# Kernel tuning notes

Measured on AMD Instinct MI355X. Metric: run time of the kernel, lower is better.

## Reference

```python
import jax, jax.numpy as jnp
import numpy as np

NA = 100000  # number of a-type nodes (rows of adj)
NB = 100000  # number of b-type nodes (cols of adj)
NE = 1600000 # number of edges (nnz of adj)
BF = 128     # b_features
AF = 128     # a_features


def setup_inputs() -> dict:
    key = jax.random.key(0)
    k1, k2, k3, k4, k5, k6 = jax.random.split(key, 6)
    stdv = 1.0 / np.sqrt(BF)
    return {
        "b_input": jax.random.normal(k1, (NB, BF), dtype=jnp.float32),
        "edge_rows": jax.random.randint(k2, (NE,), 0, NA, dtype=jnp.int32),
        "edge_cols": jax.random.randint(k3, (NE,), 0, NB, dtype=jnp.int32),
        "edge_vals": jax.random.uniform(k4, (NE,), dtype=jnp.float32),
        "a_weight": jax.random.uniform(k5, (BF, AF), minval=-stdv, maxval=stdv, dtype=jnp.float32),
        "a_bias": jax.random.uniform(k6, (AF,), minval=-stdv, maxval=stdv, dtype=jnp.float32),
    }


def reference(b_input, edge_rows, edge_cols, edge_vals, a_weight, a_bias):
    # a_support = b_input @ a_weight            : [NB, AF]
    a_support = jnp.matmul(b_input, a_weight)
    # a_output = spmm(adj, a_support)           : [NA, AF]
    # adj[r, c] = edge_vals at (edge_rows, edge_cols)
    gathered = a_support[edge_cols] * edge_vals[:, None]   # [NE, AF]
    a_output = jax.ops.segment_sum(gathered, edge_rows, num_segments=NA)
    # bias=True -> early return of a-side output
    return a_output + a_bias
```

## Files before the change

kernel.cpp:

```cpp
#include <hip/hip_runtime.h>
#include <hip/hip_bf16.h>

#define AF 128
#define BF 128
#define BROWS 64
#define CAP_F 1600
#define SORT_CAP 2048
#define CROWS 1024
#define CAP_C 18432
#define CHUNK1 2048
#define NCOARSE_MAX 128

typedef __attribute__((ext_vector_type(8))) short bf16x8;
typedef __attribute__((ext_vector_type(4))) float f32x4;

__device__ inline unsigned short f2bf(float f) {
    unsigned int u = __float_as_uint(f);
    u += 0x7FFF + ((u >> 16) & 1);
    return (unsigned short)(u >> 16);
}
__device__ inline unsigned int pk2bf(float x, float y) {
    __hip_bfloat162 h = __float22bfloat162_rn(make_float2(x, y));
    return *(unsigned int*)&h;
}
__device__ inline float bflo(unsigned int u) { return __uint_as_float(u << 16); }
__device__ inline float bfhi(unsigned int u) { return __uint_as_float(u & 0xFFFF0000u); }

__global__ __launch_bounds__(256) void prep_kernel(const float* __restrict__ W,
                                                   unsigned short* __restrict__ Wt,
                                                   int* __restrict__ grelC,
                                                   int* __restrict__ grelF) {
    const int idx = blockIdx.x * 256 + threadIdx.x;
    const int n = idx >> 7, k = idx & 127;
    Wt[idx] = f2bf(W[(size_t)k * AF + n]);
    if (blockIdx.x == 0) {
        #pragma unroll
        for (int i = threadIdx.x; i < 1024; i += 256) grelC[i] = 0;
        #pragma unroll
        for (int i = threadIdx.x; i < 2048; i += 256) grelF[i] = 0;
    }
}

__global__ __launch_bounds__(256) void phase1_kernel(const float* __restrict__ Bin,
                                                     const unsigned short* __restrict__ Wt,
                                                     unsigned int* __restrict__ Sup, int NB,
                                                     const int* __restrict__ rows,
                                                     const int* __restrict__ cols,
                                                     const float* __restrict__ vals,
                                                     int* __restrict__ grelC,
                                                     int2* __restrict__ binnedC,
                                                     int NE, int NCOARSE, int ngemm) {
    __shared__ int h[NCOARSE_MAX];
    __shared__ int rbase[NCOARSE_MAX];
    const int tid = threadIdx.x;

    if ((int)blockIdx.x < ngemm) {
        const int lane = tid & 63;
        const int wave = tid >> 6;
        const int row0 = blockIdx.x * 64;
        const int m = lane & 15;
        const int quad = lane >> 4;

        int arow = row0 + wave * 16 + m;
        int arow_c = (arow < NB) ? arow : (NB - 1);
        const float* ap = Bin + (size_t)arow_c * BF + quad * 8;
        bf16x8 af[4];
        #pragma unroll
        for (int ks = 0; ks < 4; ks++) {
            float4 lo = *(const float4*)(ap + ks * 32);
            float4 hi = *(const float4*)(ap + ks * 32 + 4);
            union { unsigned int u[4]; bf16x8 v; } cv;
            cv.u[0] = pk2bf(lo.x, lo.y); cv.u[1] = pk2bf(lo.z, lo.w);
            cv.u[2] = pk2bf(hi.x, hi.y); cv.u[3] = pk2bf(hi.z, hi.w);
            af[ks] = cv.v;
        }

        f32x4 acc[8];
        #pragma unroll
        for (int nt = 0; nt < 8; nt++) {
            f32x4 a = {0.f, 0.f, 0.f, 0.f};
            const unsigned short* wp = Wt + (size_t)(nt * 16 + m) * 128 + quad * 8;
            #pragma unroll
            for (int ks = 0; ks < 4; ks++) {
                bf16x8 bf = *(const bf16x8*)(wp + ks * 32);
                a = __builtin_amdgcn_mfma_f32_16x16x32_bf16(af[ks], bf, a, 0, 0, 0);
            }
            acc[nt] = a;
        }
        #pragma unroll
        for (int nt = 0; nt < 4; nt++) {
            #pragma unroll
            for (int r = 0; r < 4; r++) {
                int row = row0 + wave * 16 + quad * 4 + r;
                if (row < NB)
                    Sup[(size_t)row * 64 + nt * 16 + m] = pk2bf(acc[nt][r], acc[nt + 4][r]);
            }
        }
    } else {
        int bid = blockIdx.x - ngemm;
        int base = bid * CHUNK1;
        int ke[8]; int px[8]; float pv[8];
        #pragma unroll
        for (int i = 0; i < 8; i++) {
            int e = base + tid + i * 256;
            if (e < NE) {
                int r = rows[e];
                ke[i] = r >> 10;
                px[i] = cols[e] | ((r & 1023) << 17);
                pv[i] = vals[e];
            } else ke[i] = -1;
        }
        if (tid < NCOARSE) h[tid] = 0;
        __syncthreads();
        #pragma unroll
        for (int i = 0; i < 8; i++)
            if (ke[i] >= 0) atomicAdd(&h[ke[i]], 1);
        __syncthreads();
        if (tid < NCOARSE) {
            int c = h[tid];
            rbase[tid] = tid * CAP_C + (c ? atomicAdd(&grelC[tid], c) : 0);
            h[tid] = 0;
        }
        __syncthreads();
        #pragma unroll
        for (int i = 0; i < 8; i++) {
            if (ke[i] >= 0) {
                int lp = atomicAdd(&h[ke[i]], 1);
                binnedC[rbase[ke[i]] + lp] = make_int2(px[i], __float_as_int(pv[i]));
            }
        }
    }
}

__global__ __launch_bounds__(256) void passA2_kernel(const int2* __restrict__ binnedC,
                                                     const int* __restrict__ grelC,
                                                     int* __restrict__ grelF,
                                                     int2* __restrict__ binnedF, int NBUCK) {
    __shared__ int h[16];
    __shared__ int rb[16];
    const int tid = threadIdx.x;
    const int j = blockIdx.x >> 4;
    const int s = blockIdx.x & 15;
    int n = grelC[j]; if (n > CAP_C) n = CAP_C;
    const int st = (n * s) >> 4;
    const int en = (n * (s + 1)) >> 4;
    const int2* src = binnedC + (size_t)j * CAP_C;

    int sub[5]; int qx[5]; int qy[5];
    #pragma unroll
    for (int i = 0; i < 5; i++) {
        int idx = st + tid + i * 256;
        if (idx < en) {
            int2 p = src[idx];
            sub[i] = p.x >> 23;
            qx[i] = p.x & 0x7FFFFF;
            qy[i] = p.y;
        } else sub[i] = -1;
    }
    if (tid < 16) h[tid] = 0;
    __syncthreads();
    #pragma unroll
    for (int i = 0; i < 5; i++)
        if (sub[i] >= 0) atomicAdd(&h[sub[i]], 1);
    __syncthreads();
    if (tid < 16) {
        int c = h[tid];
        int fine = j * 16 + tid;
        rb[tid] = (fine < NBUCK) ? (fine * CAP_F + (c ? atomicAdd(&grelF[fine], c) : 0)) : 0;
        h[tid] = 0;
    }
    __syncthreads();
    #pragma unroll
    for (int i = 0; i < 5; i++) {
        if (sub[i] >= 0) {
            int lp = atomicAdd(&h[sub[i]], 1);
            binnedF[(size_t)rb[sub[i]] + lp] = make_int2(qx[i], qy[i]);
        }
    }
}

__global__ __launch_bounds__(256) void spmm_sorted_kernel(const unsigned short* __restrict__ Sup,
                                                          const int2* __restrict__ binned,
                                                          const int* __restrict__ grel,
                                                          const float* __restrict__ bias,
                                                          float* __restrict__ out, int NA) {
    __shared__ int2 spxy[SORT_CAP];
    __shared__ int cnt[BROWS];
    __shared__ int rs[BROWS + 1];
    __shared__ int cur[BROWS];
    const int tid = threadIdx.x;
    const int b = blockIdx.x;
    int n = grel[b]; if (n > CAP_F) n = CAP_F;
    const int2* src = binned + (size_t)b * CAP_F;

    int2 pr[7];
    #pragma unroll
    for (int j = 0; j < 7; j++) {
        int i = tid + j * 256;
        pr[j] = (i < n) ? src[i] : make_int2(-1, 0);
    }
    if (tid < BROWS) cnt[tid] = 0;
    __syncthreads();
    #pragma unroll
    for (int j = 0; j < 7; j++)
        if (pr[j].x >= 0) atomicAdd(&cnt[(pr[j].x >> 17) & 63], 1);
    __syncthreads();
    if (tid < 64) {
        int v = (cnt[tid] + 7) & ~7;
        int x = v;
        #pragma unroll
        for (int off = 1; off < 64; off <<= 1) {
            int t = __shfl_up(x, off);
            if (tid >= off) x += t;
        }
        rs[tid] = x - v;
        cur[tid] = x - v;
        if (tid == 63) rs[64] = x;
    }
    __syncthreads();
    #pragma unroll
    for (int j = 0; j < 7; j++) {
        if (pr[j].x >= 0) {
            int lr = (pr[j].x >> 17) & 63;
            int pos = atomicAdd(&cur[lr], 1);
            spxy[pos] = make_int2(pr[j].x & 0x1FFFF, pr[j].y);
        }
    }
    __syncthreads();
    if (tid < BROWS) {
        int end = rs[tid + 1];
        for (int p = cur[tid]; p < end; p++) spxy[p] = make_int2(0, 0);
    }
    __syncthreads();

    const int lane = tid & 63;
    const int wv = tid >> 6;
    const float b0 = bias[lane];
    const float b1 = bias[64 + lane];
    int r = wv * 16;
    const int rend = r + 16;
    int e = rs[r];
    const int eend = rs[rend];
    int nb = rs[r + 1];
    float ax = 0.f, ay = 0.f;

    int2 q[8]; unsigned int su[8];
    if (e < eend) {
        #pragma unroll
        for (int t = 0; t < 8; t++) q[t] = spxy[e + t];
        #pragma unroll
        for (int t = 0; t < 8; t++)
            su[t] = *(const unsigned int*)(Sup + (size_t)q[t].x * AF + lane * 2);
    }
    while (e < eend) {
        const int en2 = e + 8;
        int2 q2[8]; unsigned int s2[8];
        if (en2 < eend) {
            #pragma unroll
            for (int t = 0; t < 8; t++) q2[t] = spxy[en2 + t];
            #pragma unroll
            for (int t = 0; t < 8; t++)
                s2[t] = *(const unsigned int*)(Sup + (size_t)q2[t].x * AF + lane * 2);
        }
        while (e >= nb) {
            int row = b * BROWS + r;
            if (row < NA) {
                out[(size_t)row * AF + lane]      = ax + b0;
                out[(size_t)row * AF + 64 + lane] = ay + b1;
            }
            ax = 0.f; ay = 0.f;
            ++r; nb = rs[r + 1];
        }
        #pragma unroll
        for (int t = 0; t < 8; t++) {
            float v = __int_as_float(q[t].y);
            ax += v * bflo(su[t]);
            ay += v * bfhi(su[t]);
        }
        #pragma unroll
        for (int t = 0; t < 8; t++) { q[t] = q2[t]; su[t] = s2[t]; }
        e = en2;
    }
    while (r < rend) {
        int row = b * BROWS + r;
        if (row < NA) {
            out[(size_t)row * AF + lane]      = ax + b0;
            out[(size_t)row * AF + 64 + lane] = ay + b1;
        }
        ax = 0.f; ay = 0.f;
        ++r;
    }
}

extern "C" void kernel_launch(void* const* d_in, const int* in_sizes, int n_in,
                              void* d_out, int out_size, void* d_ws, size_t ws_size,
                              hipStream_t stream) {
    const float* b_input   = (const float*)d_in[0];
    const int*   edge_rows = (const int*)d_in[1];
    const int*   edge_cols = (const int*)d_in[2];
    const float* edge_vals = (const float*)d_in[3];
    const float* a_weight  = (const float*)d_in[4];
    const float* a_bias    = (const float*)d_in[5];
    const int NB = in_sizes[0] / BF;
    const int NE = in_sizes[1];
    const int NA = out_size / AF;
    const int NBUCK = (NA + BROWS - 1) / BROWS;
    const int NCOARSE = (NA + CROWS - 1) / CROWS;
    float* out = (float*)d_out;

    char* ws = (char*)d_ws;
    size_t off = 0;
    unsigned short* Sup = (unsigned short*)(ws + off); off += (size_t)NB * AF * sizeof(unsigned short);
    int* grelC = (int*)(ws + off); off += 1024 * sizeof(int);
    int* grelF = (int*)(ws + off); off += 2048 * sizeof(int);
    unsigned short* Wt = (unsigned short*)(ws + off); off += (size_t)128 * 128 * sizeof(unsigned short);
    int2* binnedC = (int2*)(ws + off); off += (size_t)NCOARSE * CAP_C * sizeof(int2);
    int2* binnedF = (int2*)(ws + off); off += (size_t)NBUCK * CAP_F * sizeof(int2);
    (void)ws_size; (void)n_in;

    const int ngemm = (NB + 63) / 64;
    const int npass = (NE + CHUNK1 - 1) / CHUNK1;
    prep_kernel<<<64, 256, 0, stream>>>(a_weight, Wt, grelC, grelF);
    phase1_kernel<<<ngemm + npass, 256, 0, stream>>>(
        b_input, Wt, (unsigned int*)Sup, NB,
        edge_rows, edge_cols, edge_vals, grelC, binnedC, NE, NCOARSE, ngemm);
    passA2_kernel<<<NCOARSE * 16, 256, 0, stream>>>(binnedC, grelC, grelF, binnedF, NBUCK);
    spmm_sorted_kernel<<<NBUCK, 256, 0, stream>>>(Sup, binnedF, grelF, a_bias, out, NA);
}
```

Measured before the change: 226.1 us.

## Replace two-level edge binning with direct per-row atomic slot buckets

Instead of bucketing edges in two passes (coarse buckets, then fine 64-row buckets) and sorting them in shared memory, each edge now takes a slot in a fixed-capacity per-row buffer through a global atomic on a per-row counter. This removes the second binning kernel and the in-block counting sort. The SpMM kernel then loads each row's slots directly and accumulates eight rows per wave. In exchange it adds one global atomic per edge and reads full fixed-size row buffers even when they are mostly empty. Any edges beyond 46 per row are silently dropped.

```diff
diff --git a/kernel.cpp b/kernel.cpp
--- a/kernel.cpp
+++ b/kernel.cpp
@@ -3,13 +3,10 @@
 
 #define AF 128
 #define BF 128
-#define BROWS 64
-#define CAP_F 1600
-#define SORT_CAP 2048
-#define CROWS 1024
-#define CAP_C 18432
+#define RPB 32
+#define CAP_R 46
+#define LBUF (RPB * CAP_R)
 #define CHUNK1 2048
-#define NCOARSE_MAX 128
 
 typedef __attribute__((ext_vector_type(8))) short bf16x8;
 typedef __attribute__((ext_vector_type(4))) float f32x4;
@@ -28,17 +25,13 @@
 
 __global__ __launch_bounds__(256) void prep_kernel(const float* __restrict__ W,
                                                    unsigned short* __restrict__ Wt,
-                                                   int* __restrict__ grelC,
-                                                   int* __restrict__ grelF) {
+                                                   int* __restrict__ rowcnt, int NR) {
     const int idx = blockIdx.x * 256 + threadIdx.x;
-    const int n = idx >> 7, k = idx & 127;
-    Wt[idx] = f2bf(W[(size_t)k * AF + n]);
-    if (blockIdx.x == 0) {
-        #pragma unroll
-        for (int i = threadIdx.x; i < 1024; i += 256) grelC[i] = 0;
-        #pragma unroll
-        for (int i = threadIdx.x; i < 2048; i += 256) grelF[i] = 0;
+    if (idx < 16384) {
+        const int n = idx >> 7, k = idx & 127;
+        Wt[idx] = f2bf(W[(size_t)k * AF + n]);
     }
+    for (int i = idx; i < NR; i += 32768) rowcnt[i] = 0;
 }
 
 __global__ __launch_bounds__(256) void phase1_kernel(const float* __restrict__ Bin,
@@ -47,11 +40,9 @@
                                                      const int* __restrict__ rows,
                                                      const int* __restrict__ cols,
                                                      const float* __restrict__ vals,
-                                                     int* __restrict__ grelC,
-                                                     int2* __restrict__ binnedC,
-                                                     int NE, int NCOARSE, int ngemm) {
-    __shared__ int h[NCOARSE_MAX];
-    __shared__ int rbase[NCOARSE_MAX];
+                                                     int* __restrict__ rowcnt,
+                                                     int2* __restrict__ rowbuf,
+                                                     int NE, int ngemm) {
     const int tid = threadIdx.x;
 
     if ((int)blockIdx.x < ngemm) {
@@ -97,139 +88,42 @@
             }
         }
     } else {
-        int bid = blockIdx.x - ngemm;
-        int base = bid * CHUNK1;
-        int ke[8]; int px[8]; float pv[8];
+        int base = (blockIdx.x - ngemm) * CHUNK1;
         #pragma unroll
         for (int i = 0; i < 8; i++) {
             int e = base + tid + i * 256;
             if (e < NE) {
                 int r = rows[e];
-                ke[i] = r >> 10;
-                px[i] = cols[e] | ((r & 1023) << 17);
-                pv[i] = vals[e];
-            } else ke[i] = -1;
-        }
-        if (tid < NCOARSE) h[tid] = 0;
-        __syncthreads();
-        #pragma unroll
-        for (int i = 0; i < 8; i++)
-            if (ke[i] >= 0) atomicAdd(&h[ke[i]], 1);
-        __syncthreads();
-        if (tid < NCOARSE) {
-            int c = h[tid];
-            rbase[tid] = tid * CAP_C + (c ? atomicAdd(&grelC[tid], c) : 0);
-            h[tid] = 0;
-        }
-        __syncthreads();
-        #pragma unroll
-        for (int i = 0; i < 8; i++) {
-            if (ke[i] >= 0) {
-                int lp = atomicAdd(&h[ke[i]], 1);
-                binnedC[rbase[ke[i]] + lp] = make_int2(px[i], __float_as_int(pv[i]));
+                int c = cols[e];
+                float v = vals[e];
+                int lp = atomicAdd(&rowcnt[r], 1);
+                if (lp < CAP_R)
+                    rowbuf[(size_t)r * CAP_R + lp] = make_int2(c, __float_as_int(v));
             }
         }
     }
 }
 
-__global__ __launch_bounds__(256) void passA2_kernel(const int2* __restrict__ binnedC,
-                                                     const int* __restrict__ grelC,
-                                                     int* __restrict__ grelF,
-                                                     int2* __restrict__ binnedF, int NBUCK) {
-    __shared__ int h[16];
-    __shared__ int rb[16];
-    const int tid = threadIdx.x;
-    const int j = blockIdx.x >> 4;
-    const int s = blockIdx.x & 15;
-    int n = grelC[j]; if (n > CAP_C) n = CAP_C;
-    const int st = (n * s) >> 4;
-    const int en = (n * (s + 1)) >> 4;
-    const int2* src = binnedC + (size_t)j * CAP_C;
-
-    int sub[5]; int qx[5]; int qy[5];
-    #pragma unroll
-    for (int i = 0; i < 5; i++) {
-        int idx = st + tid + i * 256;
-        if (idx < en) {
-            int2 p = src[idx];
-            sub[i] = p.x >> 23;
-            qx[i] = p.x & 0x7FFFFF;
-            qy[i] = p.y;
-        } else sub[i] = -1;
-    }
-    if (tid < 16) h[tid] = 0;
-    __syncthreads();
-    #pragma unroll
-    for (int i = 0; i < 5; i++)
-        if (sub[i] >= 0) atomicAdd(&h[sub[i]], 1);
-    __syncthreads();
-    if (tid < 16) {
-        int c = h[tid];
-        int fine = j * 16 + tid;
-        rb[tid] = (fine < NBUCK) ? (fine * CAP_F + (c ? atomicAdd(&grelF[fine], c) : 0)) : 0;
-        h[tid] = 0;
-    }
-    __syncthreads();
-    #pragma unroll
-    for (int i = 0; i < 5; i++) {
-        if (sub[i] >= 0) {
-            int lp = atomicAdd(&h[sub[i]], 1);
-            binnedF[(size_t)rb[sub[i]] + lp] = make_int2(qx[i], qy[i]);
-        }
-    }
-}
-
-__global__ __launch_bounds__(256) void spmm_sorted_kernel(const unsigned short* __restrict__ Sup,
-                                                          const int2* __restrict__ binned,
-                                                          const int* __restrict__ grel,
+__global__ __launch_bounds__(256) void spmm_direct_kernel(const unsigned short* __restrict__ Sup,
+                                                          const int2* __restrict__ rowbuf,
+                                                          const int* __restrict__ rowcnt,
                                                           const float* __restrict__ bias,
                                                           float* __restrict__ out, int NA) {
-    __shared__ int2 spxy[SORT_CAP];
-    __shared__ int cnt[BROWS];
-    __shared__ int rs[BROWS + 1];
-    __shared__ int cur[BROWS];
+    __shared__ int2 lbuf[LBUF];
+    __shared__ int lcnt[RPB];
     const int tid = threadIdx.x;
     const int b = blockIdx.x;
-    int n = grel[b]; if (n > CAP_F) n = CAP_F;
-    const int2* src = binned + (size_t)b * CAP_F;
 
-    int2 pr[7];
+    const int2* src = rowbuf + (size_t)b * LBUF;
     #pragma unroll
-    for (int j = 0; j < 7; j++) {
+    for (int j = 0; j < 6; j++) {
         int i = tid + j * 256;
-        pr[j] = (i < n) ? src[i] : make_int2(-1, 0);
+        if (i < LBUF) lbuf[i] = src[i];
     }
-    if (tid < BROWS) cnt[tid] = 0;
-    __syncthreads();
-    #pragma unroll
-    for (int j = 0; j < 7; j++)
-        if (pr[j].x >= 0) atomicAdd(&cnt[(pr[j].x >> 17) & 63], 1);
-    __syncthreads();
-    if (tid < 64) {
-        int v = (cnt[tid] + 7) & ~7;
-        int x = v;
-        #pragma unroll
-        for (int off = 1; off < 64; off <<= 1) {
-            int t = __shfl_up(x, off);
-            if (tid >= off) x += t;
-        }
-        rs[tid] = x - v;
-        cur[tid] = x - v;
-        if (tid == 63) rs[64] = x;
-    }
-    __syncthreads();
-    #pragma unroll
-    for (int j = 0; j < 7; j++) {
-        if (pr[j].x >= 0) {
-            int lr = (pr[j].x >> 17) & 63;
-            int pos = atomicAdd(&cur[lr], 1);
-            spxy[pos] = make_int2(pr[j].x & 0x1FFFF, pr[j].y);
-        }
-    }
-    __syncthreads();
-    if (tid < BROWS) {
-        int end = rs[tid + 1];
-        for (int p = cur[tid]; p < end; p++) spxy[p] = make_int2(0, 0);
+    if (tid < RPB) {
+        int gr = b * RPB + tid;
+        int c = (gr < NA) ? rowcnt[gr] : 0;
+        lcnt[tid] = (c > CAP_R) ? CAP_R : c;
     }
     __syncthreads();
 
@@ -237,58 +131,35 @@
     const int wv = tid >> 6;
     const float b0 = bias[lane];
     const float b1 = bias[64 + lane];
-    int r = wv * 16;
-    const int rend = r + 16;
-    int e = rs[r];
-    const int eend = rs[rend];
-    int nb = rs[r + 1];
-    float ax = 0.f, ay = 0.f;
 
-    int2 q[8]; unsigned int su[8];
-    if (e < eend) {
-        #pragma unroll
-        for (int t = 0; t < 8; t++) q[t] = spxy[e + t];
-        #pragma unroll
-        for (int t = 0; t < 8; t++)
-            su[t] = *(const unsigned int*)(Sup + (size_t)q[t].x * AF + lane * 2);
-    }
-    while (e < eend) {
-        const int en2 = e + 8;
-        int2 q2[8]; unsigned int s2[8];
-        if (en2 < eend) {
+    for (int r = wv * 8; r < wv * 8 + 8; ++r) {
+        int row = b * RPB + r;
+        int cnt = lcnt[r];
+        float ax = 0.f, ay = 0.f;
+        const int rb = r * CAP_R;
+        for (int e = 0; e < cnt; e += 8) {
+            int2 q[8];
             #pragma unroll
-            for (int t = 0; t < 8; t++) q2[t] = spxy[en2 + t];
+            for (int t = 0; t < 8; t++) {
+                int slot = e + t;
+                int2 p = lbuf[rb + ((slot < cnt) ? slot : 0)];
+                q[t] = (slot < cnt) ? p : make_int2(p.x, 0);
+            }
+            unsigned int su[8];
             #pragma unroll
             for (int t = 0; t < 8; t++)
-                s2[t] = *(const unsigned int*)(Sup + (size_t)q2[t].x * AF + lane * 2);
+                su[t] = *(const unsigned int*)(Sup + (size_t)q[t].x * AF + lane * 2);
+            #pragma unroll
+            for (int t = 0; t < 8; t++) {
+                float v = __int_as_float(q[t].y);
+                ax += v * bflo(su[t]);
+                ay += v * bfhi(su[t]);
+            }
         }
-        while (e >= nb) {
-            int row = b * BROWS + r;
-            if (row < NA) {
-                out[(size_t)row * AF + lane]      = ax + b0;
-                out[(size_t)row * AF + 64 + lane] = ay + b1;
-            }
-            ax = 0.f; ay = 0.f;
-            ++r; nb = rs[r + 1];
-        }
-        #pragma unroll
-        for (int t = 0; t < 8; t++) {
-            float v = __int_as_float(q[t].y);
-            ax += v * bflo(su[t]);
-            ay += v * bfhi(su[t]);
-        }
-        #pragma unroll
-        for (int t = 0; t < 8; t++) { q[t] = q2[t]; su[t] = s2[t]; }
-        e = en2;
-    }
-    while (r < rend) {
-        int row = b * BROWS + r;
         if (row < NA) {
             out[(size_t)row * AF + lane]      = ax + b0;
             out[(size_t)row * AF + 64 + lane] = ay + b1;
         }
-        ax = 0.f; ay = 0.f;
-        ++r;
     }
 }
 
@@ -304,26 +175,23 @@
     const int NB = in_sizes[0] / BF;
     const int NE = in_sizes[1];
     const int NA = out_size / AF;
-    const int NBUCK = (NA + BROWS - 1) / BROWS;
-    const int NCOARSE = (NA + CROWS - 1) / CROWS;
+    const int NBUCK = (NA + RPB - 1) / RPB;
+    const int NR = NBUCK * RPB;
     float* out = (float*)d_out;
 
     char* ws = (char*)d_ws;
     size_t off = 0;
     unsigned short* Sup = (unsigned short*)(ws + off); off += (size_t)NB * AF * sizeof(unsigned short);
-    int* grelC = (int*)(ws + off); off += 1024 * sizeof(int);
-    int* grelF = (int*)(ws + off); off += 2048 * sizeof(int);
-    unsigned short* Wt = (unsigned short*)(ws + off); off += (size_t)128 * 128 * sizeof(unsigned short);
-    int2* binnedC = (int2*)(ws + off); off += (size_t)NCOARSE * CAP_C * sizeof(int2);
-    int2* binnedF = (int2*)(ws + off); off += (size_t)NBUCK * CAP_F * sizeof(int2);
+    unsigned short* Wt  = (unsigned short*)(ws + off); off += (size_t)128 * 128 * sizeof(unsigned short);
+    int* rowcnt = (int*)(ws + off); off += (size_t)NR * sizeof(int);
+    int2* rowbuf = (int2*)(ws + off); off += (size_t)NR * CAP_R * sizeof(int2);
     (void)ws_size; (void)n_in;
 
     const int ngemm = (NB + 63) / 64;
     const int npass = (NE + CHUNK1 - 1) / CHUNK1;
-    prep_kernel<<<64, 256, 0, stream>>>(a_weight, Wt, grelC, grelF);
+    prep_kernel<<<128, 256, 0, stream>>>(a_weight, Wt, rowcnt, NR);
     phase1_kernel<<<ngemm + npass, 256, 0, stream>>>(
         b_input, Wt, (unsigned int*)Sup, NB,
-        edge_rows, edge_cols, edge_vals, grelC, binnedC, NE, NCOARSE, ngemm);
-    passA2_kernel<<<NCOARSE * 16, 256, 0, stream>>>(binnedC, grelC, grelF, binnedF, NBUCK);
-    spmm_sorted_kernel<<<NBUCK, 256, 0, stream>>>(Sup, binnedF, grelF, a_bias, out, NA);
+        edge_rows, edge_cols, edge_vals, rowcnt, rowbuf, NE, ngemm);
+    spmm_direct_kernel<<<NBUCK, 256, 0, stream>>>(Sup, rowbuf, rowcnt, a_bias, out, NA);
 }
```

Measured after the change: 275.4 us. +21.8%, slower.
